# Performance work log

Measured on AMD Instinct MI355X. Metric: run time of the kernel, lower is better.

The kernel has to match this reference:

```python
import jax, jax.numpy as jnp
import numpy as np

B, S, D, E, H, K = 4, 2048, 1024, 8, 4096, 2


def setup_inputs() -> dict:
    key = jax.random.key(0)
    ks = jax.random.split(key, 6)
    scale_in = 0.02  # keep logits/activations in a sane range
    return {
        "x": jax.random.normal(ks[0], (B, S, D), jnp.float32),
        "gate_w": jax.random.normal(ks[1], (D, E), jnp.float32) * scale_in,
        "noise_weight": jnp.zeros((E,), jnp.float32),  # torch init: zeros
        "noise": jax.random.normal(ks[2], (B, S, E), jnp.float32),
        "w1": jax.random.normal(ks[3], (E, D, H), jnp.float32) * scale_in,
        "b1": jnp.zeros((E, H), jnp.float32),
        "w2": jax.random.normal(ks[4], (E, D, H), jnp.float32) * scale_in,
        "b2": jnp.zeros((E, H), jnp.float32),
        "wp": jax.random.normal(ks[5], (E, H, D), jnp.float32) * scale_in,
        "bp": jnp.zeros((E, D), jnp.float32),
    }


def _moe(x, gate_w, noise_weight, noise, w1, b1, w2, b2, wp, bp):
    b, s, d = x.shape
    # --- noisy top-k gate ---
    logits = jnp.einsum("bsd,de->bse", x, gate_w)          # [B,S,E]
    logits_noisy = logits + noise * noise_weight            # noisy_std = 1.0
    top_v, top_i = jax.lax.top_k(logits_noisy, K)           # [B,S,K]
    # softmax over sparse logits (-inf elsewhere) == softmax over the top-k values
    probs_k = jax.nn.softmax(top_v, axis=-1)                # [B,S,K]
    onehot = jax.nn.one_hot(top_i, E, dtype=x.dtype)        # [B,S,K,E]
    gated = jnp.einsum("bsk,bske->bse", probs_k, onehot)    # [B,S,E]

    # --- dispatch / expert SwiGLU / weighted combine ---
    xf = x.reshape(b * s, d)                                # [T,D]
    gf = gated.reshape(b * s, E).T                          # [E,T]

    def body(acc, p):
        w1e, b1e, w2e, b2e, wpe, bpe, ge = p
        h = (xf @ w1e + b1e) * jax.nn.silu(xf @ w2e + b2e)  # [T,H] SwiGLU
        out = h @ wpe + bpe                                 # [T,D]
        return acc + ge[:, None] * out, None

    acc, _ = jax.lax.scan(body, jnp.zeros_like(xf), (w1, b1, w2, b2, wp, bp, gf))
    return acc.reshape(b, s, d)


def reference(x, gate_w, noise_weight, noise, w1, b1, w2, b2, wp, bp):
    return _moe(x, gate_w, noise_weight, noise, w1, b1, w2, b2, wp, bp)
```

## Files before the change

kernel.cpp:

```cpp
#include <hip/hip_runtime.h>


#define T_TOK 8192
#define DDIM 1024
#define EEXP 8
#define HDIM 4096
#define RMAX 17408

typedef short short8 __attribute__((ext_vector_type(8)));
typedef float f32x4 __attribute__((ext_vector_type(4)));
typedef unsigned short ushort4v __attribute__((ext_vector_type(4)));
typedef unsigned int u32;

__device__ __forceinline__ unsigned short f2bf(float f) {
  unsigned u = __builtin_bit_cast(unsigned, f);
  return (unsigned short)((u + 0x7FFFu + ((u >> 16) & 1u)) >> 16);
}
__device__ __forceinline__ float bf2f(unsigned short b) {
  unsigned u = ((unsigned)b) << 16;
  return __builtin_bit_cast(float, u);
}
__device__ __forceinline__ void gl_lds16(const void* g, void* l) {
  __builtin_amdgcn_global_load_lds((const u32 __attribute__((address_space(1)))*)g,
                                   (u32 __attribute__((address_space(3)))*)l, 16, 0, 0);
}

__global__ void k_convert_x(const float* __restrict__ x, unsigned short* __restrict__ xb) {
  int i = blockIdx.x * 256 + threadIdx.x;
  float4 v = ((const float4*)x)[i];
  ushort4v o;
  o.x = f2bf(v.x); o.y = f2bf(v.y); o.z = f2bf(v.z); o.w = f2bf(v.w);
  *(ushort4v*)(xb + (size_t)i * 4) = o;
}

__global__ void k_convert_w(const float* __restrict__ src, unsigned short* __restrict__ dst,
                            int N, int K) {
  __shared__ float lbuf[64 * 129];
  int e = blockIdx.z, ct = blockIdx.x, kt = blockIdx.y;
  int tid = threadIdx.x;
  const float* s = src + (size_t)e * K * N + (size_t)(kt * 64) * N + ct * 128;
#pragma unroll
  for (int q = 0; q < 8; q++) {
    int idx = q * 256 + tid;
    int row = idx >> 5, c4 = (idx & 31) * 4;
    float4 v = *(const float4*)(s + (size_t)row * N + c4);
    lbuf[row * 129 + c4 + 0] = v.x;
    lbuf[row * 129 + c4 + 1] = v.y;
    lbuf[row * 129 + c4 + 2] = v.z;
    lbuf[row * 129 + c4 + 3] = v.w;
  }
  __syncthreads();
  unsigned short* dt = dst + ((size_t)(e * (N / 128) + ct) * (K / 64) + kt) * 8192;
#pragma unroll
  for (int q = 0; q < 4; q++) {
    int idx = q * 256 + tid;
    int kc = idx & 7, n = idx >> 3;
    short8 o;
#pragma unroll
    for (int j = 0; j < 8; j++) o[j] = (short)f2bf(lbuf[(kc * 8 + j) * 129 + n]);
    int byte = (n * 128 + kc * 16) ^ ((n & 7) << 4);
    *(short8*)((char*)dt + byte) = o;
  }
}

__global__ void k_init(int* __restrict__ rowtok, int* __restrict__ counts, int* __restrict__ cursor) {
  int i = blockIdx.x * 256 + threadIdx.x;
  if (i < RMAX) rowtok[i] = 0;
  if (i < EEXP) { counts[i] = 0; cursor[i] = 0; }
}

__launch_bounds__(256)
__global__ void k_gate(const float* __restrict__ x, const float* __restrict__ gw,
                       const float* __restrict__ nwt, const float* __restrict__ noi,
                       int* __restrict__ tki, float* __restrict__ tkp,
                       int* __restrict__ counts) {
  __shared__ float gwT[8][1024];
  int tid = threadIdx.x;
#pragma unroll
  for (int q = 0; q < 32; q++) {
    int flat = q * 256 + tid;
    gwT[flat & 7][flat >> 3] = gw[flat];
  }
  __syncthreads();
  int wave = tid >> 6, l = tid & 63;
  int t = blockIdx.x * 4 + wave;
  float acc[8] = {0.f, 0.f, 0.f, 0.f, 0.f, 0.f, 0.f, 0.f};
  const float4* xr = (const float4*)(x + (size_t)t * DDIM);
#pragma unroll
  for (int i = 0; i < 4; i++) {
    float4 xv = xr[l + i * 64];
    int d0 = (l + i * 64) * 4;
#pragma unroll
    for (int e = 0; e < 8; e++) {
      float4 gv = *(const float4*)&gwT[e][d0];
      acc[e] += xv.x * gv.x + xv.y * gv.y + xv.z * gv.z + xv.w * gv.w;
    }
  }
#pragma unroll
  for (int s = 1; s < 64; s <<= 1) {
#pragma unroll
    for (int e = 0; e < 8; e++) acc[e] += __shfl_xor(acc[e], s, 64);
  }
  if (l == 0) {
    float nl[8];
#pragma unroll
    for (int e = 0; e < 8; e++) nl[e] = acc[e] + noi[t * 8 + e] * nwt[e];
    int i0 = 0; float v0 = nl[0];
#pragma unroll
    for (int e = 1; e < 8; e++) if (nl[e] > v0) { v0 = nl[e]; i0 = e; }
    int i1 = -1; float v1 = -3.4e38f;
#pragma unroll
    for (int e = 0; e < 8; e++) if (e != i0 && nl[e] > v1) { v1 = nl[e]; i1 = e; }
    float ex = __expf(v1 - v0);
    float p0 = 1.f / (1.f + ex);
    float p1 = ex * p0;
    tki[2 * t] = i0; tki[2 * t + 1] = i1;
    tkp[2 * t] = p0; tkp[2 * t + 1] = p1;
    atomicAdd(&counts[i0], 1);
    atomicAdd(&counts[i1], 1);
  }
}

__global__ void k_prefix(const int* __restrict__ counts, int* __restrict__ basep) {
  if (threadIdx.x == 0) {
    int b = 0;
    for (int e = 0; e < EEXP; e++) { basep[e] = b; b += (counts[e] + 127) & ~127; }
  }
}

__global__ void k_scatter(const int* __restrict__ tki, const int* __restrict__ basep,
                          int* __restrict__ cursor, int* __restrict__ rowtok,
                          int* __restrict__ t2r) {
  int t = blockIdx.x * 256 + threadIdx.x;
  if (t >= T_TOK) return;
#pragma unroll
  for (int k = 0; k < 2; k++) {
    int e = tki[2 * t + k];
    int pos = atomicAdd(&cursor[e], 1);
    int row = basep[e] + pos;
    rowtok[row] = t;
    t2r[2 * t + k] = row;
  }
}

__launch_bounds__(256, 2)
__global__ void k_gemm1(const unsigned short* __restrict__ xb,
                        const unsigned short* __restrict__ w1s, const unsigned short* __restrict__ w2s,
                        const float* __restrict__ b1g, const float* __restrict__ b2g,
                        const int* __restrict__ counts, const int* __restrict__ basep,
                        const int* __restrict__ rowtok,
                        unsigned short* __restrict__ hout) {
  int e = blockIdx.y >> 6;
  int rt = blockIdx.y & 63;
  int cnt = counts[e];
  if (rt >= ((cnt + 127) >> 7)) return;
  int ct = blockIdx.x;
  int row0 = basep[e] + rt * 128;
  int col0 = ct * 128;

  __shared__ char smem[49152];
  __shared__ int s_tok[128];
  __shared__ float s_b1[128], s_b2[128];

  int tid = threadIdx.x;
  if (tid < 128) {
    s_tok[tid] = rowtok[row0 + tid];
    s_b1[tid] = b1g[e * HDIM + col0 + tid];
    s_b2[tid] = b2g[e * HDIM + col0 + tid];
  }
  __syncthreads();

  int wave = tid >> 6, l = tid & 63;
  int wr = (wave >> 1) << 6, wc = (wave & 1) << 6;
  int g = l >> 4, ln = l & 15;

  int sr[4], stok[4], sxor[4];
#pragma unroll
  for (int q = 0; q < 4; q++) {
    int flat = q * 256 + tid;
    sr[q] = flat;
    int r = flat >> 3, c = flat & 7;
    stok[q] = s_tok[r];
    sxor[q] = (c ^ (r & 7)) << 3;
  }

  f32x4 zero = {0.f, 0.f, 0.f, 0.f};
  f32x4 acc_a[4][4], acc_b[4][4];
#pragma unroll
  for (int m = 0; m < 4; m++)
#pragma unroll
    for (int n = 0; n < 4; n++) { acc_a[m][n] = zero; acc_b[m][n] = zero; }

  const unsigned short* w1t = w1s + ((size_t)(e * 32 + ct) * 16) * 8192;
  const unsigned short* w2t = w2s + ((size_t)(e * 32 + ct) * 16) * 8192;

  for (int kt = 0; kt < 16; kt++) {
#pragma unroll
    for (int q = 0; q < 4; q++) {
      gl_lds16(xb + (size_t)stok[q] * DDIM + kt * 64 + sxor[q], smem + sr[q] * 16);
      gl_lds16(w1t + (size_t)kt * 8192 + sr[q] * 8, smem + 16384 + sr[q] * 16);
      gl_lds16(w2t + (size_t)kt * 8192 + sr[q] * 8, smem + 32768 + sr[q] * 16);
    }
    __syncthreads();
#pragma unroll
    for (int ks = 0; ks < 2; ks++) {
      int kb = ks * 64 + g * 16;
      short8 af[4], bf1[4], bf2[4];
#pragma unroll
      for (int m = 0; m < 4; m++) {
        int r = wr + m * 16 + ln;
        af[m] = *(const short8*)(smem + ((r * 128 + kb) ^ ((r & 7) << 4)));
      }
#pragma unroll
      for (int n = 0; n < 4; n++) {
        int r = wc + n * 16 + ln;
        int byte = (r * 128 + kb) ^ ((r & 7) << 4);
        bf1[n] = *(const short8*)(smem + 16384 + byte);
        bf2[n] = *(const short8*)(smem + 32768 + byte);
      }
#pragma unroll
      for (int m = 0; m < 4; m++)
#pragma unroll
        for (int n = 0; n < 4; n++) {
          acc_a[m][n] = __builtin_amdgcn_mfma_f32_16x16x32_bf16(af[m], bf1[n], acc_a[m][n], 0, 0, 0);
          acc_b[m][n] = __builtin_amdgcn_mfma_f32_16x16x32_bf16(af[m], bf2[n], acc_b[m][n], 0, 0, 0);
        }
    }
    __syncthreads();
  }
  unsigned short* ht = (unsigned short*)smem;
#pragma unroll
  for (int m = 0; m < 4; m++)
#pragma unroll
    for (int n = 0; n < 4; n++)
#pragma unroll
      for (int r = 0; r < 4; r++) {
        int row = wr + m * 16 + g * 4 + r;
        int col = wc + n * 16 + ln;
        float a = acc_a[m][n][r] + s_b1[col];
        float b = acc_b[m][n][r] + s_b2[col];
        float hv = a * (b / (1.f + __expf(-b)));
        ht[row * 128 + col] = f2bf(hv);
      }
  __syncthreads();
#pragma unroll
  for (int q = 0; q < 8; q++) {
    int idx = q * 256 + tid;
    int row = idx >> 4, chunk = idx & 15;
    short8 v = *(const short8*)(smem + idx * 16);
    *(short8*)(hout + (size_t)(row0 + row) * HDIM + col0 + chunk * 8) = v;
  }
}

__launch_bounds__(256, 2)
__global__ void k_gemm2(const unsigned short* __restrict__ hin,
                        const unsigned short* __restrict__ wps, const float* __restrict__ bpg,
                        const int* __restrict__ counts, const int* __restrict__ basep,
                        unsigned short* __restrict__ yout) {
  int e = blockIdx.y >> 6;
  int rt = blockIdx.y & 63;
  int cnt = counts[e];
  if (rt >= ((cnt + 127) >> 7)) return;
  int ct = blockIdx.x;
  int row0 = basep[e] + rt * 128;
  int col0 = ct * 128;

  __shared__ char smem[32768];
  __shared__ float s_bp[128];
  int tid = threadIdx.x;
  if (tid < 128) s_bp[tid] = bpg[e * DDIM + col0 + tid];
  __syncthreads();

  int wave = tid >> 6, l = tid & 63;
  int wr = (wave >> 1) << 6, wc = (wave & 1) << 6;
  int g = l >> 4, ln = l & 15;

  int sr[4], srow[4], sxor[4];
#pragma unroll
  for (int q = 0; q < 4; q++) {
    int flat = q * 256 + tid;
    sr[q] = flat;
    int r = flat >> 3, c = flat & 7;
    srow[q] = row0 + r;
    sxor[q] = (c ^ (r & 7)) << 3;
  }

  f32x4 zero = {0.f, 0.f, 0.f, 0.f};
  f32x4 acc[4][4];
#pragma unroll
  for (int m = 0; m < 4; m++)
#pragma unroll
    for (int n = 0; n < 4; n++) acc[m][n] = zero;

  const unsigned short* wpt = wps + ((size_t)(e * 8 + ct) * 64) * 8192;

  for (int kt = 0; kt < 64; kt++) {
#pragma unroll
    for (int q = 0; q < 4; q++) {
      gl_lds16(hin + (size_t)srow[q] * HDIM + kt * 64 + sxor[q], smem + sr[q] * 16);
      gl_lds16(wpt + (size_t)kt * 8192 + sr[q] * 8, smem + 16384 + sr[q] * 16);
    }
    __syncthreads();
#pragma unroll
    for (int ks = 0; ks < 2; ks++) {
      int kb = ks * 64 + g * 16;
      short8 af[4], bf[4];
#pragma unroll
      for (int m = 0; m < 4; m++) {
        int r = wr + m * 16 + ln;
        af[m] = *(const short8*)(smem + ((r * 128 + kb) ^ ((r & 7) << 4)));
      }
#pragma unroll
      for (int n = 0; n < 4; n++) {
        int r = wc + n * 16 + ln;
        bf[n] = *(const short8*)(smem + 16384 + ((r * 128 + kb) ^ ((r & 7) << 4)));
      }
#pragma unroll
      for (int m = 0; m < 4; m++)
#pragma unroll
        for (int n = 0; n < 4; n++)
          acc[m][n] = __builtin_amdgcn_mfma_f32_16x16x32_bf16(af[m], bf[n], acc[m][n], 0, 0, 0);
    }
    __syncthreads();
  }
  unsigned short* ht = (unsigned short*)smem;
#pragma unroll
  for (int m = 0; m < 4; m++)
#pragma unroll
    for (int n = 0; n < 4; n++)
#pragma unroll
      for (int r = 0; r < 4; r++) {
        int row = wr + m * 16 + g * 4 + r;
        int col = wc + n * 16 + ln;
        ht[row * 128 + col] = f2bf(acc[m][n][r] + s_bp[col]);
      }
  __syncthreads();
#pragma unroll
  for (int q = 0; q < 8; q++) {
    int idx = q * 256 + tid;
    int row = idx >> 4, chunk = idx & 15;
    short8 v = *(const short8*)(smem + idx * 16);
    *(short8*)(yout + (size_t)(row0 + row) * DDIM + col0 + chunk * 8) = v;
  }
}

__global__ void k_combine(const unsigned short* __restrict__ yv,
                          const int* __restrict__ t2r, const float* __restrict__ tkp,
                          float* __restrict__ outp) {
  int gid = blockIdx.x * 256 + threadIdx.x;
  int t = gid >> 8;
  int c4 = (gid & 255) << 2;
  int r0 = t2r[2 * t], r1 = t2r[2 * t + 1];
  float p0 = tkp[2 * t], p1 = tkp[2 * t + 1];
  ushort4v u0 = *(const ushort4v*)(yv + (size_t)r0 * DDIM + c4);
  ushort4v u1 = *(const ushort4v*)(yv + (size_t)r1 * DDIM + c4);
  float4 o;
  o.x = p0 * bf2f(u0.x) + p1 * bf2f(u1.x);
  o.y = p0 * bf2f(u0.y) + p1 * bf2f(u1.y);
  o.z = p0 * bf2f(u0.z) + p1 * bf2f(u1.z);
  o.w = p0 * bf2f(u0.w) + p1 * bf2f(u1.w);
  *(float4*)(outp + (size_t)t * DDIM + c4) = o;
}

extern "C" void kernel_launch(void* const* d_in, const int* in_sizes, int n_in,
                              void* d_out, int out_size, void* d_ws, size_t ws_size,
                              hipStream_t stream) {
  const float* x   = (const float*)d_in[0];
  const float* gw  = (const float*)d_in[1];
  const float* nwt = (const float*)d_in[2];
  const float* noi = (const float*)d_in[3];
  const float* w1  = (const float*)d_in[4];
  const float* b1  = (const float*)d_in[5];
  const float* w2  = (const float*)d_in[6];
  const float* b2  = (const float*)d_in[7];
  const float* wp  = (const float*)d_in[8];
  const float* bp  = (const float*)d_in[9];
  float* outp = (float*)d_out;
  char* ws = (char*)d_ws;

  constexpr size_t SZ_W = (size_t)EEXP * DDIM * HDIM * 2;
  constexpr size_t OFF_XB  = 0;
  constexpr size_t OFF_W1S = OFF_XB + (size_t)T_TOK * DDIM * 2;
  constexpr size_t OFF_W2S = OFF_W1S + SZ_W;
  constexpr size_t OFF_WPS = OFF_W2S + SZ_W;
  constexpr size_t OFF_H   = OFF_WPS + SZ_W;
  constexpr size_t OFF_Y   = OFF_H + (size_t)RMAX * HDIM * 2;
  constexpr size_t OFF_RT  = OFF_Y + (size_t)RMAX * DDIM * 2;
  constexpr size_t OFF_TKI = OFF_RT + (size_t)RMAX * 4;
  constexpr size_t OFF_TKP = OFF_TKI + (size_t)T_TOK * 2 * 4;
  constexpr size_t OFF_T2R = OFF_TKP + (size_t)T_TOK * 2 * 4;
  constexpr size_t OFF_CNT = OFF_T2R + (size_t)T_TOK * 2 * 4;
  constexpr size_t OFF_BAS = OFF_CNT + 256;
  constexpr size_t OFF_CUR = OFF_BAS + 256;

  unsigned short* xb  = (unsigned short*)(ws + OFF_XB);
  unsigned short* w1s = (unsigned short*)(ws + OFF_W1S);
  unsigned short* w2s = (unsigned short*)(ws + OFF_W2S);
  unsigned short* wps = (unsigned short*)(ws + OFF_WPS);
  unsigned short* h   = (unsigned short*)(ws + OFF_H);
  unsigned short* y   = (unsigned short*)(ws + OFF_Y);
  int*   rowtok = (int*)(ws + OFF_RT);
  int*   tki    = (int*)(ws + OFF_TKI);
  float* tkp    = (float*)(ws + OFF_TKP);
  int*   t2r    = (int*)(ws + OFF_T2R);
  int*   counts = (int*)(ws + OFF_CNT);
  int*   basep  = (int*)(ws + OFF_BAS);
  int*   cursor = (int*)(ws + OFF_CUR);

  dim3 blk(256);
  k_convert_x<<<dim3((T_TOK * DDIM / 4) / 256), blk, 0, stream>>>(x, xb);
  k_init<<<dim3((RMAX + 255) / 256), blk, 0, stream>>>(rowtok, counts, cursor);
  k_gate<<<dim3(T_TOK / 4), blk, 0, stream>>>(x, gw, nwt, noi, tki, tkp, counts);
  k_convert_w<<<dim3(HDIM / 128, DDIM / 64, EEXP), blk, 0, stream>>>(w1, w1s, HDIM, DDIM);
  k_convert_w<<<dim3(HDIM / 128, DDIM / 64, EEXP), blk, 0, stream>>>(w2, w2s, HDIM, DDIM);
  k_convert_w<<<dim3(DDIM / 128, HDIM / 64, EEXP), blk, 0, stream>>>(wp, wps, DDIM, HDIM);
  k_prefix<<<dim3(1), dim3(64), 0, stream>>>(counts, basep);
  k_scatter<<<dim3(T_TOK / 256), blk, 0, stream>>>(tki, basep, cursor, rowtok, t2r);
  k_gemm1<<<dim3(HDIM / 128, EEXP * 64), blk, 0, stream>>>(xb, w1s, w2s, b1, b2, counts, basep, rowtok, h);
  k_gemm2<<<dim3(DDIM / 128, EEXP * 64), blk, 0, stream>>>(h, wps, bp, counts, basep, y);
  k_combine<<<dim3(T_TOK), blk, 0, stream>>>(y, t2r, tkp, outp);
  (void)in_sizes; (void)n_in; (void)out_size; (void)ws_size;
}
```

Before: 932.3 us.

## Enlarge GEMM tiles to 512 threads, double-buffer LDS, fuse x conversion into gate

Result: slower. 1.081 ms (+15.9%).

```diff
diff --git a/kernel.cpp b/kernel.cpp
--- a/kernel.cpp
+++ b/kernel.cpp
@@ -5,7 +5,7 @@
 #define DDIM 1024
 #define EEXP 8
 #define HDIM 4096
-#define RMAX 17408
+#define RMAX 18432
 
 typedef short short8 __attribute__((ext_vector_type(8)));
 typedef float f32x4 __attribute__((ext_vector_type(4)));
@@ -23,14 +23,6 @@
 __device__ __forceinline__ void gl_lds16(const void* g, void* l) {
   __builtin_amdgcn_global_load_lds((const u32 __attribute__((address_space(1)))*)g,
                                    (u32 __attribute__((address_space(3)))*)l, 16, 0, 0);
-}
-
-__global__ void k_convert_x(const float* __restrict__ x, unsigned short* __restrict__ xb) {
-  int i = blockIdx.x * 256 + threadIdx.x;
-  float4 v = ((const float4*)x)[i];
-  ushort4v o;
-  o.x = f2bf(v.x); o.y = f2bf(v.y); o.z = f2bf(v.z); o.w = f2bf(v.w);
-  *(ushort4v*)(xb + (size_t)i * 4) = o;
 }
 
 __global__ void k_convert_w(const float* __restrict__ src, unsigned short* __restrict__ dst,
@@ -73,7 +65,7 @@
 __global__ void k_gate(const float* __restrict__ x, const float* __restrict__ gw,
                        const float* __restrict__ nwt, const float* __restrict__ noi,
                        int* __restrict__ tki, float* __restrict__ tkp,
-                       int* __restrict__ counts) {
+                       int* __restrict__ counts, unsigned short* __restrict__ xb) {
   __shared__ float gwT[8][1024];
   int tid = threadIdx.x;
 #pragma unroll
@@ -90,6 +82,9 @@
   for (int i = 0; i < 4; i++) {
     float4 xv = xr[l + i * 64];
     int d0 = (l + i * 64) * 4;
+    ushort4v o;
+    o.x = f2bf(xv.x); o.y = f2bf(xv.y); o.z = f2bf(xv.z); o.w = f2bf(xv.w);
+    *(ushort4v*)(xb + (size_t)t * DDIM + d0) = o;
 #pragma unroll
     for (int e = 0; e < 8; e++) {
       float4 gv = *(const float4*)&gwT[e][d0];
@@ -124,7 +119,7 @@
 __global__ void k_prefix(const int* __restrict__ counts, int* __restrict__ basep) {
   if (threadIdx.x == 0) {
     int b = 0;
-    for (int e = 0; e < EEXP; e++) { basep[e] = b; b += (counts[e] + 127) & ~127; }
+    for (int e = 0; e < EEXP; e++) { basep[e] = b; b += (counts[e] + 255) & ~255; }
   }
 }
 
@@ -143,7 +138,7 @@
   }
 }
 
-__launch_bounds__(256, 2)
+__launch_bounds__(512, 2)
 __global__ void k_gemm1(const unsigned short* __restrict__ xb,
                         const unsigned short* __restrict__ w1s, const unsigned short* __restrict__ w2s,
                         const float* __restrict__ b1g, const float* __restrict__ b2g,
@@ -153,90 +148,102 @@
   int e = blockIdx.y >> 6;
   int rt = blockIdx.y & 63;
   int cnt = counts[e];
-  if (rt >= ((cnt + 127) >> 7)) return;
+  if (rt >= ((cnt + 255) >> 8)) return;
   int ct = blockIdx.x;
-  int row0 = basep[e] + rt * 128;
+  int row0 = basep[e] + rt * 256;
   int col0 = ct * 128;
 
-  __shared__ char smem[49152];
-  __shared__ int s_tok[128];
+  __shared__ char smem[131072];
+  __shared__ int s_tok[256];
   __shared__ float s_b1[128], s_b2[128];
 
   int tid = threadIdx.x;
+  if (tid < 256) s_tok[tid] = rowtok[row0 + tid];
   if (tid < 128) {
-    s_tok[tid] = rowtok[row0 + tid];
     s_b1[tid] = b1g[e * HDIM + col0 + tid];
     s_b2[tid] = b2g[e * HDIM + col0 + tid];
   }
   __syncthreads();
 
   int wave = tid >> 6, l = tid & 63;
-  int wr = (wave >> 1) << 6, wc = (wave & 1) << 6;
+  int wm = wave >> 2, wn = wave & 3;
   int g = l >> 4, ln = l & 15;
 
-  int sr[4], stok[4], sxor[4];
+  size_t a_src[4]; int a_dst[4];
 #pragma unroll
   for (int q = 0; q < 4; q++) {
-    int flat = q * 256 + tid;
-    sr[q] = flat;
-    int r = flat >> 3, c = flat & 7;
-    stok[q] = s_tok[r];
-    sxor[q] = (c ^ (r & 7)) << 3;
+    int c = q * 512 + tid;
+    int r = c >> 3, cc = (c & 7) ^ (r & 7);
+    a_src[q] = (size_t)s_tok[r] * (DDIM * 2) + cc * 16;
+    a_dst[q] = c * 16;
   }
 
   f32x4 zero = {0.f, 0.f, 0.f, 0.f};
-  f32x4 acc_a[4][4], acc_b[4][4];
-#pragma unroll
-  for (int m = 0; m < 4; m++)
-#pragma unroll
-    for (int n = 0; n < 4; n++) { acc_a[m][n] = zero; acc_b[m][n] = zero; }
-
-  const unsigned short* w1t = w1s + ((size_t)(e * 32 + ct) * 16) * 8192;
-  const unsigned short* w2t = w2s + ((size_t)(e * 32 + ct) * 16) * 8192;
-
+  f32x4 acc_a[8][2], acc_b[8][2];
+#pragma unroll
+  for (int m = 0; m < 8; m++)
+#pragma unroll
+    for (int n = 0; n < 2; n++) { acc_a[m][n] = zero; acc_b[m][n] = zero; }
+
+  const char* xbb = (const char*)xb;
+  const char* w1t = (const char*)(w1s + ((size_t)(e * 32 + ct) * 16) * 8192);
+  const char* w2t = (const char*)(w2s + ((size_t)(e * 32 + ct) * 16) * 8192);
+
+#define STAGE1(buf, kt)                                                          \
+  {                                                                              \
+    int _kt = (kt);                                                              \
+    _Pragma("unroll") for (int q = 0; q < 4; q++)                                \
+      gl_lds16(xbb + a_src[q] + _kt * 128, smem + (buf) * 32768 + a_dst[q]);     \
+    _Pragma("unroll") for (int q = 0; q < 2; q++) {                              \
+      int c = q * 512 + tid;                                                     \
+      gl_lds16(w1t + (size_t)_kt * 16384 + c * 16, smem + 65536 + (buf) * 16384 + c * 16); \
+      gl_lds16(w2t + (size_t)_kt * 16384 + c * 16, smem + 98304 + (buf) * 16384 + c * 16); \
+    }                                                                            \
+  }
+
+  STAGE1(0, 0);
+  __syncthreads();
+
+  int cur = 0;
   for (int kt = 0; kt < 16; kt++) {
-#pragma unroll
-    for (int q = 0; q < 4; q++) {
-      gl_lds16(xb + (size_t)stok[q] * DDIM + kt * 64 + sxor[q], smem + sr[q] * 16);
-      gl_lds16(w1t + (size_t)kt * 8192 + sr[q] * 8, smem + 16384 + sr[q] * 16);
-      gl_lds16(w2t + (size_t)kt * 8192 + sr[q] * 8, smem + 32768 + sr[q] * 16);
-    }
-    __syncthreads();
+    if (kt < 15) STAGE1(cur ^ 1, kt + 1);
 #pragma unroll
     for (int ks = 0; ks < 2; ks++) {
       int kb = ks * 64 + g * 16;
-      short8 af[4], bf1[4], bf2[4];
-#pragma unroll
-      for (int m = 0; m < 4; m++) {
-        int r = wr + m * 16 + ln;
-        af[m] = *(const short8*)(smem + ((r * 128 + kb) ^ ((r & 7) << 4)));
-      }
-#pragma unroll
-      for (int n = 0; n < 4; n++) {
-        int r = wc + n * 16 + ln;
+      short8 af[8], bf1[2], bf2[2];
+#pragma unroll
+      for (int m = 0; m < 8; m++) {
+        int r = wm * 128 + m * 16 + ln;
+        af[m] = *(const short8*)(smem + cur * 32768 + ((r * 128 + kb) ^ ((r & 7) << 4)));
+      }
+#pragma unroll
+      for (int n = 0; n < 2; n++) {
+        int r = wn * 32 + n * 16 + ln;
         int byte = (r * 128 + kb) ^ ((r & 7) << 4);
-        bf1[n] = *(const short8*)(smem + 16384 + byte);
-        bf2[n] = *(const short8*)(smem + 32768 + byte);
-      }
-#pragma unroll
-      for (int m = 0; m < 4; m++)
-#pragma unroll
-        for (int n = 0; n < 4; n++) {
+        bf1[n] = *(const short8*)(smem + 65536 + cur * 16384 + byte);
+        bf2[n] = *(const short8*)(smem + 98304 + cur * 16384 + byte);
+      }
+#pragma unroll
+      for (int m = 0; m < 8; m++)
+#pragma unroll
+        for (int n = 0; n < 2; n++) {
           acc_a[m][n] = __builtin_amdgcn_mfma_f32_16x16x32_bf16(af[m], bf1[n], acc_a[m][n], 0, 0, 0);
           acc_b[m][n] = __builtin_amdgcn_mfma_f32_16x16x32_bf16(af[m], bf2[n], acc_b[m][n], 0, 0, 0);
         }
     }
     __syncthreads();
-  }
+    cur ^= 1;
+  }
+
   unsigned short* ht = (unsigned short*)smem;
 #pragma unroll
-  for (int m = 0; m < 4; m++)
-#pragma unroll
-    for (int n = 0; n < 4; n++)
+  for (int m = 0; m < 8; m++)
+#pragma unroll
+    for (int n = 0; n < 2; n++)
 #pragma unroll
       for (int r = 0; r < 4; r++) {
-        int row = wr + m * 16 + g * 4 + r;
-        int col = wc + n * 16 + ln;
+        int row = wm * 128 + m * 16 + g * 4 + r;
+        int col = wn * 32 + n * 16 + ln;
         float a = acc_a[m][n][r] + s_b1[col];
         float b = acc_b[m][n][r] + s_b2[col];
         float hv = a * (b / (1.f + __expf(-b)));
@@ -245,14 +252,14 @@
   __syncthreads();
 #pragma unroll
   for (int q = 0; q < 8; q++) {
-    int idx = q * 256 + tid;
-    int row = idx >> 4, chunk = idx & 15;
+    int idx = q * 512 + tid;
+    int row = idx >> 4, cc = (idx & 15) * 8;
     short8 v = *(const short8*)(smem + idx * 16);
-    *(short8*)(hout + (size_t)(row0 + row) * HDIM + col0 + chunk * 8) = v;
-  }
-}
-
-__launch_bounds__(256, 2)
+    *(short8*)(hout + (size_t)(row0 + row) * HDIM + col0 + cc) = v;
+  }
+}
+
+__launch_bounds__(512, 2)
 __global__ void k_gemm2(const unsigned short* __restrict__ hin,
                         const unsigned short* __restrict__ wps, const float* __restrict__ bpg,
                         const int* __restrict__ counts, const int* __restrict__ basep,
@@ -263,26 +270,25 @@
   if (rt >= ((cnt + 127) >> 7)) return;
   int ct = blockIdx.x;
   int row0 = basep[e] + rt * 128;
-  int col0 = ct * 128;
-
-  __shared__ char smem[32768];
-  __shared__ float s_bp[128];
+  int col0 = ct * 256;
+
+  __shared__ char smem[98304];
+  __shared__ float s_bp[256];
   int tid = threadIdx.x;
-  if (tid < 128) s_bp[tid] = bpg[e * DDIM + col0 + tid];
+  if (tid < 256) s_bp[tid] = bpg[e * DDIM + col0 + tid];
   __syncthreads();
 
   int wave = tid >> 6, l = tid & 63;
-  int wr = (wave >> 1) << 6, wc = (wave & 1) << 6;
+  int wm = wave >> 2, wn = wave & 3;
   int g = l >> 4, ln = l & 15;
 
-  int sr[4], srow[4], sxor[4];
-#pragma unroll
-  for (int q = 0; q < 4; q++) {
-    int flat = q * 256 + tid;
-    sr[q] = flat;
-    int r = flat >> 3, c = flat & 7;
-    srow[q] = row0 + r;
-    sxor[q] = (c ^ (r & 7)) << 3;
+  size_t a_src[2]; int a_dst[2];
+#pragma unroll
+  for (int q = 0; q < 2; q++) {
+    int c = q * 512 + tid;
+    int r = c >> 3, cc = (c & 7) ^ (r & 7);
+    a_src[q] = (size_t)(row0 + r) * (HDIM * 2) + cc * 16;
+    a_dst[q] = c * 16;
   }
 
   f32x4 zero = {0.f, 0.f, 0.f, 0.f};
@@ -292,28 +298,43 @@
 #pragma unroll
     for (int n = 0; n < 4; n++) acc[m][n] = zero;
 
-  const unsigned short* wpt = wps + ((size_t)(e * 8 + ct) * 64) * 8192;
-
+  const char* hb = (const char*)hin;
+  const char* wpt = (const char*)(wps + ((size_t)(e * 8 + ct * 2) * 64) * 8192);
+
+#define STAGE2(buf, kt)                                                          \
+  {                                                                              \
+    int _kt = (kt);                                                              \
+    _Pragma("unroll") for (int q = 0; q < 2; q++)                                \
+      gl_lds16(hb + a_src[q] + _kt * 128, smem + (buf) * 16384 + a_dst[q]);      \
+    _Pragma("unroll") for (int q = 0; q < 4; q++) {                              \
+      int c = q * 512 + tid;                                                     \
+      int sub = c >> 10;                                                         \
+      gl_lds16(wpt + (size_t)(sub * 64 + _kt) * 16384 + (c & 1023) * 16,         \
+               smem + 32768 + (buf) * 32768 + c * 16);                           \
+    }                                                                            \
+  }
+
+  STAGE2(0, 0);
+  __syncthreads();
+
+  int cur = 0;
   for (int kt = 0; kt < 64; kt++) {
-#pragma unroll
-    for (int q = 0; q < 4; q++) {
-      gl_lds16(hin + (size_t)srow[q] * HDIM + kt * 64 + sxor[q], smem + sr[q] * 16);
-      gl_lds16(wpt + (size_t)kt * 8192 + sr[q] * 8, smem + 16384 + sr[q] * 16);
-    }
-    __syncthreads();
+    if (kt < 63) STAGE2(cur ^ 1, kt + 1);
 #pragma unroll
     for (int ks = 0; ks < 2; ks++) {
       int kb = ks * 64 + g * 16;
       short8 af[4], bf[4];
 #pragma unroll
       for (int m = 0; m < 4; m++) {
-        int r = wr + m * 16 + ln;
-        af[m] = *(const short8*)(smem + ((r * 128 + kb) ^ ((r & 7) << 4)));
+        int r = wm * 64 + m * 16 + ln;
+        af[m] = *(const short8*)(smem + cur * 16384 + ((r * 128 + kb) ^ ((r & 7) << 4)));
       }
 #pragma unroll
       for (int n = 0; n < 4; n++) {
-        int r = wc + n * 16 + ln;
-        bf[n] = *(const short8*)(smem + 16384 + ((r * 128 + kb) ^ ((r & 7) << 4)));
+        int rg = wn * 64 + n * 16 + ln;
+        int sub = rg >> 7, rr = rg & 127;
+        bf[n] = *(const short8*)(smem + 32768 + cur * 32768 + sub * 16384 +
+                                 ((rr * 128 + kb) ^ ((rr & 7) << 4)));
       }
 #pragma unroll
       for (int m = 0; m < 4; m++)
@@ -322,7 +343,9 @@
           acc[m][n] = __builtin_amdgcn_mfma_f32_16x16x32_bf16(af[m], bf[n], acc[m][n], 0, 0, 0);
     }
     __syncthreads();
-  }
+    cur ^= 1;
+  }
+
   unsigned short* ht = (unsigned short*)smem;
 #pragma unroll
   for (int m = 0; m < 4; m++)
@@ -330,17 +353,17 @@
     for (int n = 0; n < 4; n++)
 #pragma unroll
       for (int r = 0; r < 4; r++) {
-        int row = wr + m * 16 + g * 4 + r;
-        int col = wc + n * 16 + ln;
-        ht[row * 128 + col] = f2bf(acc[m][n][r] + s_bp[col]);
+        int row = wm * 64 + m * 16 + g * 4 + r;
+        int col = wn * 64 + n * 16 + ln;
+        ht[row * 256 + col] = f2bf(acc[m][n][r] + s_bp[col]);
       }
   __syncthreads();
 #pragma unroll
   for (int q = 0; q < 8; q++) {
-    int idx = q * 256 + tid;
-    int row = idx >> 4, chunk = idx & 15;
+    int idx = q * 512 + tid;
+    int row = idx >> 5, cc = (idx & 31) * 8;
     short8 v = *(const short8*)(smem + idx * 16);
-    *(short8*)(yout + (size_t)(row0 + row) * DDIM + col0 + chunk * 8) = v;
+    *(short8*)(yout + (size_t)(row0 + row) * DDIM + col0 + cc) = v;
   }
 }
 
@@ -408,16 +431,15 @@
   int*   cursor = (int*)(ws + OFF_CUR);
 
   dim3 blk(256);
-  k_convert_x<<<dim3((T_TOK * DDIM / 4) / 256), blk, 0, stream>>>(x, xb);
   k_init<<<dim3((RMAX + 255) / 256), blk, 0, stream>>>(rowtok, counts, cursor);
-  k_gate<<<dim3(T_TOK / 4), blk, 0, stream>>>(x, gw, nwt, noi, tki, tkp, counts);
+  k_gate<<<dim3(T_TOK / 4), blk, 0, stream>>>(x, gw, nwt, noi, tki, tkp, counts, xb);
   k_convert_w<<<dim3(HDIM / 128, DDIM / 64, EEXP), blk, 0, stream>>>(w1, w1s, HDIM, DDIM);
   k_convert_w<<<dim3(HDIM / 128, DDIM / 64, EEXP), blk, 0, stream>>>(w2, w2s, HDIM, DDIM);
   k_convert_w<<<dim3(DDIM / 128, HDIM / 64, EEXP), blk, 0, stream>>>(wp, wps, DDIM, HDIM);
   k_prefix<<<dim3(1), dim3(64), 0, stream>>>(counts, basep);
   k_scatter<<<dim3(T_TOK / 256), blk, 0, stream>>>(tki, basep, cursor, rowtok, t2r);
-  k_gemm1<<<dim3(HDIM / 128, EEXP * 64), blk, 0, stream>>>(xb, w1s, w2s, b1, b2, counts, basep, rowtok, h);
-  k_gemm2<<<dim3(DDIM / 128, EEXP * 64), blk, 0, stream>>>(h, wps, bp, counts, basep, y);
+  k_gemm1<<<dim3(HDIM / 128, EEXP * 64), dim3(512), 0, stream>>>(xb, w1s, w2s, b1, b2, counts, basep, rowtok, h);
+  k_gemm2<<<dim3(DDIM / 256, EEXP * 64), dim3(512), 0, stream>>>(h, wps, bp, counts, basep, y);
   k_combine<<<dim3(T_TOK), blk, 0, stream>>>(y, t2r, tkp, outp);
   (void)in_sizes; (void)n_in; (void)out_size; (void)ws_size;
 }
```

## Fuse combine into gemm2 via atomic scatter-add and merge conversion kernels

Applied to the files above, without the earlier changes.

After: 922.1 us. No clear change (-1.1%).

```diff
diff --git a/kernel.cpp b/kernel.cpp
--- a/kernel.cpp
+++ b/kernel.cpp
@@ -16,27 +16,36 @@
   unsigned u = __builtin_bit_cast(unsigned, f);
   return (unsigned short)((u + 0x7FFFu + ((u >> 16) & 1u)) >> 16);
 }
-__device__ __forceinline__ float bf2f(unsigned short b) {
-  unsigned u = ((unsigned)b) << 16;
-  return __builtin_bit_cast(float, u);
-}
 __device__ __forceinline__ void gl_lds16(const void* g, void* l) {
   __builtin_amdgcn_global_load_lds((const u32 __attribute__((address_space(1)))*)g,
                                    (u32 __attribute__((address_space(3)))*)l, 16, 0, 0);
 }
-
-__global__ void k_convert_x(const float* __restrict__ x, unsigned short* __restrict__ xb) {
+#define MFMA_BF16 __builtin_amdgcn_mfma_f32_16x16x32_bf16
+
+__global__ void k_init(int* __restrict__ rowtok, float* __restrict__ rowp,
+                       int* __restrict__ counts, int* __restrict__ cursor,
+                       float4* __restrict__ out4) {
   int i = blockIdx.x * 256 + threadIdx.x;
-  float4 v = ((const float4*)x)[i];
-  ushort4v o;
-  o.x = f2bf(v.x); o.y = f2bf(v.y); o.z = f2bf(v.z); o.w = f2bf(v.w);
-  *(ushort4v*)(xb + (size_t)i * 4) = o;
-}
-
-__global__ void k_convert_w(const float* __restrict__ src, unsigned short* __restrict__ dst,
-                            int N, int K) {
+  if (i < RMAX) { rowtok[i] = 0; rowp[i] = 0.f; }
+  if (i < EEXP) { counts[i] = 0; cursor[i] = 0; }
+  float4 z = {0.f, 0.f, 0.f, 0.f};
+  out4[i] = z;
+  out4[i + 1048576] = z;
+}
+
+__global__ void k_convert_all(const float* __restrict__ w1, const float* __restrict__ w2,
+                              const float* __restrict__ wp,
+                              unsigned short* __restrict__ w1s, unsigned short* __restrict__ w2s,
+                              unsigned short* __restrict__ wps) {
   __shared__ float lbuf[64 * 129];
-  int e = blockIdx.z, ct = blockIdx.x, kt = blockIdx.y;
+  int bid = blockIdx.x;
+  int seg = bid >> 12;
+  int t = bid & 4095;
+  const float* src; unsigned short* dst; int N, K, ct, kt, e;
+  e = t >> 9;
+  if (seg == 0)      { src = w1; dst = w1s; N = HDIM; K = DDIM; ct = (t >> 4) & 31; kt = t & 15; }
+  else if (seg == 1) { src = w2; dst = w2s; N = HDIM; K = DDIM; ct = (t >> 4) & 31; kt = t & 15; }
+  else               { src = wp; dst = wps; N = DDIM; K = HDIM; ct = (t >> 6) & 7;  kt = t & 63; }
   int tid = threadIdx.x;
   const float* s = src + (size_t)e * K * N + (size_t)(kt * 64) * N + ct * 128;
 #pragma unroll
@@ -63,17 +72,11 @@
   }
 }
 
-__global__ void k_init(int* __restrict__ rowtok, int* __restrict__ counts, int* __restrict__ cursor) {
-  int i = blockIdx.x * 256 + threadIdx.x;
-  if (i < RMAX) rowtok[i] = 0;
-  if (i < EEXP) { counts[i] = 0; cursor[i] = 0; }
-}
-
 __launch_bounds__(256)
 __global__ void k_gate(const float* __restrict__ x, const float* __restrict__ gw,
                        const float* __restrict__ nwt, const float* __restrict__ noi,
                        int* __restrict__ tki, float* __restrict__ tkp,
-                       int* __restrict__ counts) {
+                       int* __restrict__ counts, unsigned short* __restrict__ xb) {
   __shared__ float gwT[8][1024];
   int tid = threadIdx.x;
 #pragma unroll
@@ -90,6 +93,9 @@
   for (int i = 0; i < 4; i++) {
     float4 xv = xr[l + i * 64];
     int d0 = (l + i * 64) * 4;
+    ushort4v o;
+    o.x = f2bf(xv.x); o.y = f2bf(xv.y); o.z = f2bf(xv.z); o.w = f2bf(xv.w);
+    *(ushort4v*)(xb + (size_t)t * DDIM + d0) = o;
 #pragma unroll
     for (int e = 0; e < 8; e++) {
       float4 gv = *(const float4*)&gwT[e][d0];
@@ -128,9 +134,9 @@
   }
 }
 
-__global__ void k_scatter(const int* __restrict__ tki, const int* __restrict__ basep,
-                          int* __restrict__ cursor, int* __restrict__ rowtok,
-                          int* __restrict__ t2r) {
+__global__ void k_scatter(const int* __restrict__ tki, const float* __restrict__ tkp,
+                          const int* __restrict__ basep, int* __restrict__ cursor,
+                          int* __restrict__ rowtok, float* __restrict__ rowp) {
   int t = blockIdx.x * 256 + threadIdx.x;
   if (t >= T_TOK) return;
 #pragma unroll
@@ -139,7 +145,7 @@
     int pos = atomicAdd(&cursor[e], 1);
     int row = basep[e] + pos;
     rowtok[row] = t;
-    t2r[2 * t + k] = row;
+    rowp[row] = tkp[2 * t + k];
   }
 }
 
@@ -150,11 +156,14 @@
                         const int* __restrict__ counts, const int* __restrict__ basep,
                         const int* __restrict__ rowtok,
                         unsigned short* __restrict__ hout) {
-  int e = blockIdx.y >> 6;
-  int rt = blockIdx.y & 63;
+  int lin = blockIdx.x;
+  int orig = (lin & 7) * 2048 + (lin >> 3);
+  int ct = orig & 31;
+  int yy = orig >> 5;
+  int e = yy >> 6;
+  int rt = yy & 63;
   int cnt = counts[e];
   if (rt >= ((cnt + 127) >> 7)) return;
-  int ct = blockIdx.x;
   int row0 = basep[e] + rt * 128;
   int col0 = ct * 128;
 
@@ -222,8 +231,8 @@
       for (int m = 0; m < 4; m++)
 #pragma unroll
         for (int n = 0; n < 4; n++) {
-          acc_a[m][n] = __builtin_amdgcn_mfma_f32_16x16x32_bf16(af[m], bf1[n], acc_a[m][n], 0, 0, 0);
-          acc_b[m][n] = __builtin_amdgcn_mfma_f32_16x16x32_bf16(af[m], bf2[n], acc_b[m][n], 0, 0, 0);
+          acc_a[m][n] = MFMA_BF16(af[m], bf1[n], acc_a[m][n], 0, 0, 0);
+          acc_b[m][n] = MFMA_BF16(af[m], bf2[n], acc_b[m][n], 0, 0, 0);
         }
     }
     __syncthreads();
@@ -256,19 +265,28 @@
 __global__ void k_gemm2(const unsigned short* __restrict__ hin,
                         const unsigned short* __restrict__ wps, const float* __restrict__ bpg,
                         const int* __restrict__ counts, const int* __restrict__ basep,
-                        unsigned short* __restrict__ yout) {
-  int e = blockIdx.y >> 6;
-  int rt = blockIdx.y & 63;
+                        const int* __restrict__ rowtok, const float* __restrict__ rowp,
+                        float* __restrict__ outp) {
+  int lin = blockIdx.x;
+  int orig = (lin & 7) * 512 + (lin >> 3);
+  int ct = orig & 7;
+  int yy = orig >> 3;
+  int e = yy >> 6;
+  int rt = yy & 63;
   int cnt = counts[e];
   if (rt >= ((cnt + 127) >> 7)) return;
-  int ct = blockIdx.x;
   int row0 = basep[e] + rt * 128;
   int col0 = ct * 128;
 
   __shared__ char smem[32768];
-  __shared__ float s_bp[128];
+  __shared__ int s_tok[128];
+  __shared__ float s_p[128], s_bp[128];
   int tid = threadIdx.x;
-  if (tid < 128) s_bp[tid] = bpg[e * DDIM + col0 + tid];
+  if (tid < 128) {
+    s_tok[tid] = rowtok[row0 + tid];
+    s_p[tid] = rowp[row0 + tid];
+    s_bp[tid] = bpg[e * DDIM + col0 + tid];
+  }
   __syncthreads();
 
   int wave = tid >> 6, l = tid & 63;
@@ -319,47 +337,26 @@
       for (int m = 0; m < 4; m++)
 #pragma unroll
         for (int n = 0; n < 4; n++)
-          acc[m][n] = __builtin_amdgcn_mfma_f32_16x16x32_bf16(af[m], bf[n], acc[m][n], 0, 0, 0);
+          acc[m][n] = MFMA_BF16(af[m], bf[n], acc[m][n], 0, 0, 0);
     }
     __syncthreads();
   }
-  unsigned short* ht = (unsigned short*)smem;
+
 #pragma unroll
   for (int m = 0; m < 4; m++)
 #pragma unroll
-    for (int n = 0; n < 4; n++)
-#pragma unroll
-      for (int r = 0; r < 4; r++) {
-        int row = wr + m * 16 + g * 4 + r;
-        int col = wc + n * 16 + ln;
-        ht[row * 128 + col] = f2bf(acc[m][n][r] + s_bp[col]);
-      }
-  __syncthreads();
-#pragma unroll
-  for (int q = 0; q < 8; q++) {
-    int idx = q * 256 + tid;
-    int row = idx >> 4, chunk = idx & 15;
-    short8 v = *(const short8*)(smem + idx * 16);
-    *(short8*)(yout + (size_t)(row0 + row) * DDIM + col0 + chunk * 8) = v;
-  }
-}
-
-__global__ void k_combine(const unsigned short* __restrict__ yv,
-                          const int* __restrict__ t2r, const float* __restrict__ tkp,
-                          float* __restrict__ outp) {
-  int gid = blockIdx.x * 256 + threadIdx.x;
-  int t = gid >> 8;
-  int c4 = (gid & 255) << 2;
-  int r0 = t2r[2 * t], r1 = t2r[2 * t + 1];
-  float p0 = tkp[2 * t], p1 = tkp[2 * t + 1];
-  ushort4v u0 = *(const ushort4v*)(yv + (size_t)r0 * DDIM + c4);
-  ushort4v u1 = *(const ushort4v*)(yv + (size_t)r1 * DDIM + c4);
-  float4 o;
-  o.x = p0 * bf2f(u0.x) + p1 * bf2f(u1.x);
-  o.y = p0 * bf2f(u0.y) + p1 * bf2f(u1.y);
-  o.z = p0 * bf2f(u0.z) + p1 * bf2f(u1.z);
-  o.w = p0 * bf2f(u0.w) + p1 * bf2f(u1.w);
-  *(float4*)(outp + (size_t)t * DDIM + c4) = o;
+    for (int r = 0; r < 4; r++) {
+      int row = wr + m * 16 + g * 4 + r;
+      float p = s_p[row];
+      if (p != 0.f) {
+        size_t obase = (size_t)s_tok[row] * DDIM + col0;
+#pragma unroll
+        for (int n = 0; n < 4; n++) {
+          int col = wc + n * 16 + ln;
+          atomicAdd(&outp[obase + col], p * (acc[m][n][r] + s_bp[col]));
+        }
+      }
+    }
 }
 
 extern "C" void kernel_launch(void* const* d_in, const int* in_sizes, int n_in,
@@ -384,12 +381,11 @@
   constexpr size_t OFF_W2S = OFF_W1S + SZ_W;
   constexpr size_t OFF_WPS = OFF_W2S + SZ_W;
   constexpr size_t OFF_H   = OFF_WPS + SZ_W;
-  constexpr size_t OFF_Y   = OFF_H + (size_t)RMAX * HDIM * 2;
-  constexpr size_t OFF_RT  = OFF_Y + (size_t)RMAX * DDIM * 2;
-  constexpr size_t OFF_TKI = OFF_RT + (size_t)RMAX * 4;
+  constexpr size_t OFF_RT  = OFF_H + (size_t)RMAX * HDIM * 2;
+  constexpr size_t OFF_RP  = OFF_RT + (size_t)RMAX * 4;
+  constexpr size_t OFF_TKI = OFF_RP + (size_t)RMAX * 4;
   constexpr size_t OFF_TKP = OFF_TKI + (size_t)T_TOK * 2 * 4;
-  constexpr size_t OFF_T2R = OFF_TKP + (size_t)T_TOK * 2 * 4;
-  constexpr size_t OFF_CNT = OFF_T2R + (size_t)T_TOK * 2 * 4;
+  constexpr size_t OFF_CNT = OFF_TKP + (size_t)T_TOK * 2 * 4;
   constexpr size_t OFF_BAS = OFF_CNT + 256;
   constexpr size_t OFF_CUR = OFF_BAS + 256;
 
@@ -398,26 +394,21 @@
   unsigned short* w2s = (unsigned short*)(ws + OFF_W2S);
   unsigned short* wps = (unsigned short*)(ws + OFF_WPS);
   unsigned short* h   = (unsigned short*)(ws + OFF_H);
-  unsigned short* y   = (unsigned short*)(ws + OFF_Y);
   int*   rowtok = (int*)(ws + OFF_RT);
+  float* rowp   = (float*)(ws + OFF_RP);
   int*   tki    = (int*)(ws + OFF_TKI);
   float* tkp    = (float*)(ws + OFF_TKP);
-  int*   t2r    = (int*)(ws + OFF_T2R);
   int*   counts = (int*)(ws + OFF_CNT);
   int*   basep  = (int*)(ws + OFF_BAS);
   int*   cursor = (int*)(ws + OFF_CUR);
 
   dim3 blk(256);
-  k_convert_x<<<dim3((T_TOK * DDIM / 4) / 256), blk, 0, stream>>>(x, xb);
-  k_init<<<dim3((RMAX + 255) / 256), blk, 0, stream>>>(rowtok, counts, cursor);
-  k_gate<<<dim3(T_TOK / 4), blk, 0, stream>>>(x, gw, nwt, noi, tki, tkp, counts);
-  k_convert_w<<<dim3(HDIM / 128, DDIM / 64, EEXP), blk, 0, stream>>>(w1, w1s, HDIM, DDIM);
-  k_convert_w<<<dim3(HDIM / 128, DDIM / 64, EEXP), blk, 0, stream>>>(w2, w2s, HDIM, DDIM);
-  k_convert_w<<<dim3(DDIM / 128, HDIM / 64, EEXP), blk, 0, stream>>>(wp, wps, DDIM, HDIM);
+  k_init<<<dim3(4096), blk, 0, stream>>>(rowtok, rowp, counts, cursor, (float4*)outp);
+  k_gate<<<dim3(T_TOK / 4), blk, 0, stream>>>(x, gw, nwt, noi, tki, tkp, counts, xb);
+  k_convert_all<<<dim3(12288), blk, 0, stream>>>(w1, w2, wp, w1s, w2s, wps);
   k_prefix<<<dim3(1), dim3(64), 0, stream>>>(counts, basep);
-  k_scatter<<<dim3(T_TOK / 256), blk, 0, stream>>>(tki, basep, cursor, rowtok, t2r);
-  k_gemm1<<<dim3(HDIM / 128, EEXP * 64), blk, 0, stream>>>(xb, w1s, w2s, b1, b2, counts, basep, rowtok, h);
-  k_gemm2<<<dim3(DDIM / 128, EEXP * 64), blk, 0, stream>>>(h, wps, bp, counts, basep, y);
-  k_combine<<<dim3(T_TOK), blk, 0, stream>>>(y, t2r, tkp, outp);
+  k_scatter<<<dim3(T_TOK / 256), blk, 0, stream>>>(tki, tkp, basep, cursor, rowtok, rowp);
+  k_gemm1<<<dim3(16384), blk, 0, stream>>>(xb, w1s, w2s, b1, b2, counts, basep, rowtok, h);
+  k_gemm2<<<dim3(4096), blk, 0, stream>>>(h, wps, bp, counts, basep, rowtok, rowp, outp);
   (void)in_sizes; (void)n_in; (void)out_size; (void)ws_size;
 }
```

## Retile expert down-projection GEMM to 256x128 and fuse conversion launches

Applied to the files above, without the earlier changes.

Result: slower. 957.1 us (+2.7%).

```diff
diff --git a/kernel.cpp b/kernel.cpp
--- a/kernel.cpp
+++ b/kernel.cpp
@@ -5,7 +5,7 @@
 #define DDIM 1024
 #define EEXP 8
 #define HDIM 4096
-#define RMAX 17408
+#define RMAX 18432
 
 typedef short short8 __attribute__((ext_vector_type(8)));
 typedef float f32x4 __attribute__((ext_vector_type(4)));
@@ -24,19 +24,27 @@
   __builtin_amdgcn_global_load_lds((const u32 __attribute__((address_space(1)))*)g,
                                    (u32 __attribute__((address_space(3)))*)l, 16, 0, 0);
 }
-
-__global__ void k_convert_x(const float* __restrict__ x, unsigned short* __restrict__ xb) {
+#define MFMA_BF16 __builtin_amdgcn_mfma_f32_16x16x32_bf16
+
+__global__ void k_init(int* __restrict__ rowtok, int* __restrict__ counts, int* __restrict__ cursor) {
   int i = blockIdx.x * 256 + threadIdx.x;
-  float4 v = ((const float4*)x)[i];
-  ushort4v o;
-  o.x = f2bf(v.x); o.y = f2bf(v.y); o.z = f2bf(v.z); o.w = f2bf(v.w);
-  *(ushort4v*)(xb + (size_t)i * 4) = o;
-}
-
-__global__ void k_convert_w(const float* __restrict__ src, unsigned short* __restrict__ dst,
-                            int N, int K) {
+  if (i < RMAX) rowtok[i] = 0;
+  if (i < EEXP) { counts[i] = 0; cursor[i] = 0; }
+}
+
+__global__ void k_convert_all(const float* __restrict__ w1, const float* __restrict__ w2,
+                              const float* __restrict__ wp,
+                              unsigned short* __restrict__ w1s, unsigned short* __restrict__ w2s,
+                              unsigned short* __restrict__ wps) {
   __shared__ float lbuf[64 * 129];
-  int e = blockIdx.z, ct = blockIdx.x, kt = blockIdx.y;
+  int bid = blockIdx.x;
+  int seg = bid >> 12;
+  int t = bid & 4095;
+  const float* src; unsigned short* dst; int N, K, ct, kt, e;
+  e = t >> 9;
+  if (seg == 0)      { src = w1; dst = w1s; N = HDIM; K = DDIM; ct = (t >> 4) & 31; kt = t & 15; }
+  else if (seg == 1) { src = w2; dst = w2s; N = HDIM; K = DDIM; ct = (t >> 4) & 31; kt = t & 15; }
+  else               { src = wp; dst = wps; N = DDIM; K = HDIM; ct = (t >> 6) & 7;  kt = t & 63; }
   int tid = threadIdx.x;
   const float* s = src + (size_t)e * K * N + (size_t)(kt * 64) * N + ct * 128;
 #pragma unroll
@@ -63,17 +71,11 @@
   }
 }
 
-__global__ void k_init(int* __restrict__ rowtok, int* __restrict__ counts, int* __restrict__ cursor) {
-  int i = blockIdx.x * 256 + threadIdx.x;
-  if (i < RMAX) rowtok[i] = 0;
-  if (i < EEXP) { counts[i] = 0; cursor[i] = 0; }
-}
-
 __launch_bounds__(256)
 __global__ void k_gate(const float* __restrict__ x, const float* __restrict__ gw,
                        const float* __restrict__ nwt, const float* __restrict__ noi,
                        int* __restrict__ tki, float* __restrict__ tkp,
-                       int* __restrict__ counts) {
+                       int* __restrict__ counts, unsigned short* __restrict__ xb) {
   __shared__ float gwT[8][1024];
   int tid = threadIdx.x;
 #pragma unroll
@@ -90,6 +92,9 @@
   for (int i = 0; i < 4; i++) {
     float4 xv = xr[l + i * 64];
     int d0 = (l + i * 64) * 4;
+    ushort4v o;
+    o.x = f2bf(xv.x); o.y = f2bf(xv.y); o.z = f2bf(xv.z); o.w = f2bf(xv.w);
+    *(ushort4v*)(xb + (size_t)t * DDIM + d0) = o;
 #pragma unroll
     for (int e = 0; e < 8; e++) {
       float4 gv = *(const float4*)&gwT[e][d0];
@@ -124,7 +129,7 @@
 __global__ void k_prefix(const int* __restrict__ counts, int* __restrict__ basep) {
   if (threadIdx.x == 0) {
     int b = 0;
-    for (int e = 0; e < EEXP; e++) { basep[e] = b; b += (counts[e] + 127) & ~127; }
+    for (int e = 0; e < EEXP; e++) { basep[e] = b; b += (counts[e] + 255) & ~255; }
   }
 }
 
@@ -222,8 +227,8 @@
       for (int m = 0; m < 4; m++)
 #pragma unroll
         for (int n = 0; n < 4; n++) {
-          acc_a[m][n] = __builtin_amdgcn_mfma_f32_16x16x32_bf16(af[m], bf1[n], acc_a[m][n], 0, 0, 0);
-          acc_b[m][n] = __builtin_amdgcn_mfma_f32_16x16x32_bf16(af[m], bf2[n], acc_b[m][n], 0, 0, 0);
+          acc_a[m][n] = MFMA_BF16(af[m], bf1[n], acc_a[m][n], 0, 0, 0);
+          acc_b[m][n] = MFMA_BF16(af[m], bf2[n], acc_b[m][n], 0, 0, 0);
         }
     }
     __syncthreads();
@@ -252,33 +257,32 @@
   }
 }
 
-__launch_bounds__(256, 2)
+__launch_bounds__(512, 2)
 __global__ void k_gemm2(const unsigned short* __restrict__ hin,
                         const unsigned short* __restrict__ wps, const float* __restrict__ bpg,
                         const int* __restrict__ counts, const int* __restrict__ basep,
                         unsigned short* __restrict__ yout) {
-  int e = blockIdx.y >> 6;
-  int rt = blockIdx.y & 63;
+  int e = blockIdx.y / 33;
+  int rt = blockIdx.y % 33;
   int cnt = counts[e];
-  if (rt >= ((cnt + 127) >> 7)) return;
+  if (rt >= ((cnt + 255) >> 8)) return;
   int ct = blockIdx.x;
-  int row0 = basep[e] + rt * 128;
+  int row0 = basep[e] + rt * 256;
   int col0 = ct * 128;
 
-  __shared__ char smem[32768];
+  __shared__ char smem[49152];
   __shared__ float s_bp[128];
   int tid = threadIdx.x;
   if (tid < 128) s_bp[tid] = bpg[e * DDIM + col0 + tid];
-  __syncthreads();
 
   int wave = tid >> 6, l = tid & 63;
-  int wr = (wave >> 1) << 6, wc = (wave & 1) << 6;
+  int wm = wave >> 2, wn = wave & 3;
   int g = l >> 4, ln = l & 15;
 
   int sr[4], srow[4], sxor[4];
 #pragma unroll
   for (int q = 0; q < 4; q++) {
-    int flat = q * 256 + tid;
+    int flat = q * 512 + tid;
     sr[q] = flat;
     int r = flat >> 3, c = flat & 7;
     srow[q] = row0 + r;
@@ -286,61 +290,71 @@
   }
 
   f32x4 zero = {0.f, 0.f, 0.f, 0.f};
-  f32x4 acc[4][4];
-#pragma unroll
-  for (int m = 0; m < 4; m++)
-#pragma unroll
-    for (int n = 0; n < 4; n++) acc[m][n] = zero;
+  f32x4 acc[8][2];
+#pragma unroll
+  for (int m = 0; m < 8; m++)
+#pragma unroll
+    for (int n = 0; n < 2; n++) acc[m][n] = zero;
 
   const unsigned short* wpt = wps + ((size_t)(e * 8 + ct) * 64) * 8192;
 
   for (int kt = 0; kt < 64; kt++) {
 #pragma unroll
-    for (int q = 0; q < 4; q++) {
+    for (int q = 0; q < 4; q++)
       gl_lds16(hin + (size_t)srow[q] * HDIM + kt * 64 + sxor[q], smem + sr[q] * 16);
-      gl_lds16(wpt + (size_t)kt * 8192 + sr[q] * 8, smem + 16384 + sr[q] * 16);
+#pragma unroll
+    for (int q = 0; q < 2; q++) {
+      int f2 = q * 512 + tid;
+      gl_lds16(wpt + (size_t)kt * 8192 + f2 * 8, smem + 32768 + f2 * 16);
     }
     __syncthreads();
 #pragma unroll
     for (int ks = 0; ks < 2; ks++) {
       int kb = ks * 64 + g * 16;
-      short8 af[4], bf[4];
-#pragma unroll
-      for (int m = 0; m < 4; m++) {
-        int r = wr + m * 16 + ln;
+      short8 af[8], bf[2];
+#pragma unroll
+      for (int m = 0; m < 8; m++) {
+        int r = wm * 128 + m * 16 + ln;
         af[m] = *(const short8*)(smem + ((r * 128 + kb) ^ ((r & 7) << 4)));
       }
 #pragma unroll
-      for (int n = 0; n < 4; n++) {
-        int r = wc + n * 16 + ln;
-        bf[n] = *(const short8*)(smem + 16384 + ((r * 128 + kb) ^ ((r & 7) << 4)));
+      for (int n = 0; n < 2; n++) {
+        int r = wn * 32 + n * 16 + ln;
+        bf[n] = *(const short8*)(smem + 32768 + ((r * 128 + kb) ^ ((r & 7) << 4)));
       }
 #pragma unroll
-      for (int m = 0; m < 4; m++)
-#pragma unroll
-        for (int n = 0; n < 4; n++)
-          acc[m][n] = __builtin_amdgcn_mfma_f32_16x16x32_bf16(af[m], bf[n], acc[m][n], 0, 0, 0);
-    }
-    __syncthreads();
-  }
+      for (int m = 0; m < 8; m++)
+#pragma unroll
+        for (int n = 0; n < 2; n++)
+          acc[m][n] = MFMA_BF16(af[m], bf[n], acc[m][n], 0, 0, 0);
+    }
+    __syncthreads();
+  }
+
   unsigned short* ht = (unsigned short*)smem;
 #pragma unroll
-  for (int m = 0; m < 4; m++)
-#pragma unroll
-    for (int n = 0; n < 4; n++)
-#pragma unroll
-      for (int r = 0; r < 4; r++) {
-        int row = wr + m * 16 + g * 4 + r;
-        int col = wc + n * 16 + ln;
-        ht[row * 128 + col] = f2bf(acc[m][n][r] + s_bp[col]);
-      }
-  __syncthreads();
-#pragma unroll
-  for (int q = 0; q < 8; q++) {
-    int idx = q * 256 + tid;
-    int row = idx >> 4, chunk = idx & 15;
-    short8 v = *(const short8*)(smem + idx * 16);
-    *(short8*)(yout + (size_t)(row0 + row) * DDIM + col0 + chunk * 8) = v;
+  for (int half = 0; half < 2; half++) {
+    if (wm == half) {
+#pragma unroll
+      for (int m = 0; m < 8; m++)
+#pragma unroll
+        for (int n = 0; n < 2; n++)
+#pragma unroll
+          for (int r = 0; r < 4; r++) {
+            int lrow = m * 16 + g * 4 + r;
+            int col = wn * 32 + n * 16 + ln;
+            ht[lrow * 128 + col] = f2bf(acc[m][n][r] + s_bp[col]);
+          }
+    }
+    __syncthreads();
+#pragma unroll
+    for (int q = 0; q < 4; q++) {
+      int idx = q * 512 + tid;
+      int row = idx >> 4, cc = (idx & 15) * 8;
+      short8 v = *(const short8*)(smem + idx * 16);
+      *(short8*)(yout + (size_t)(row0 + half * 128 + row) * DDIM + col0 + cc) = v;
+    }
+    __syncthreads();
   }
 }
 
@@ -408,16 +422,13 @@
   int*   cursor = (int*)(ws + OFF_CUR);
 
   dim3 blk(256);
-  k_convert_x<<<dim3((T_TOK * DDIM / 4) / 256), blk, 0, stream>>>(x, xb);
   k_init<<<dim3((RMAX + 255) / 256), blk, 0, stream>>>(rowtok, counts, cursor);
-  k_gate<<<dim3(T_TOK / 4), blk, 0, stream>>>(x, gw, nwt, noi, tki, tkp, counts);
-  k_convert_w<<<dim3(HDIM / 128, DDIM / 64, EEXP), blk, 0, stream>>>(w1, w1s, HDIM, DDIM);
-  k_convert_w<<<dim3(HDIM / 128, DDIM / 64, EEXP), blk, 0, stream>>>(w2, w2s, HDIM, DDIM);
-  k_convert_w<<<dim3(DDIM / 128, HDIM / 64, EEXP), blk, 0, stream>>>(wp, wps, DDIM, HDIM);
+  k_gate<<<dim3(T_TOK / 4), blk, 0, stream>>>(x, gw, nwt, noi, tki, tkp, counts, xb);
+  k_convert_all<<<dim3(12288), blk, 0, stream>>>(w1, w2, wp, w1s, w2s, wps);
   k_prefix<<<dim3(1), dim3(64), 0, stream>>>(counts, basep);
   k_scatter<<<dim3(T_TOK / 256), blk, 0, stream>>>(tki, basep, cursor, rowtok, t2r);
   k_gemm1<<<dim3(HDIM / 128, EEXP * 64), blk, 0, stream>>>(xb, w1s, w2s, b1, b2, counts, basep, rowtok, h);
-  k_gemm2<<<dim3(DDIM / 128, EEXP * 64), blk, 0, stream>>>(h, wps, bp, counts, basep, y);
+  k_gemm2<<<dim3(DDIM / 128, EEXP * 33), dim3(512), 0, stream>>>(h, wps, bp, counts, basep, y);
   k_combine<<<dim3(T_TOK), blk, 0, stream>>>(y, t2r, tkp, outp);
   (void)in_sizes; (void)n_in; (void)out_size; (void)ws_size;
 }
```
